# Kernel tuning notes

Hardware: AMD Instinct MI355X
Metric: run time of the kernel (lower is better)

Reference implementation:

```python
import jax, jax.numpy as jnp
import numpy as np

DIM = 1024
NUM_HEADS = 16
NUM_KV_HEADS = 2
HEAD_DIM = DIM // NUM_HEADS          # 64
REPEATS = NUM_HEADS // NUM_KV_HEADS  # 8
WINDOW = 256
HALF = WINDOW // 2                   # 128
BATCH, SEQ = 2, 2048


def setup_inputs() -> dict:
    key = jax.random.key(0)
    ks = jax.random.split(key, 9)
    sc = 1.0 / np.sqrt(DIM)
    return {
        "x":  jax.random.normal(ks[0], (BATCH, SEQ, DIM), jnp.float32),
        "Wq": jax.random.normal(ks[1], (DIM, NUM_HEADS * HEAD_DIM), jnp.float32) * sc,
        "bq": jax.random.normal(ks[2], (NUM_HEADS * HEAD_DIM,), jnp.float32) * 0.01,
        "Wk": jax.random.normal(ks[3], (DIM, NUM_KV_HEADS * HEAD_DIM), jnp.float32) * sc,
        "bk": jax.random.normal(ks[4], (NUM_KV_HEADS * HEAD_DIM,), jnp.float32) * 0.01,
        "Wv": jax.random.normal(ks[5], (DIM, NUM_KV_HEADS * HEAD_DIM), jnp.float32) * sc,
        "bv": jax.random.normal(ks[6], (NUM_KV_HEADS * HEAD_DIM,), jnp.float32) * 0.01,
        "Wo": jax.random.normal(ks[7], (DIM, DIM), jnp.float32) * sc,
        "bo": jax.random.normal(ks[8], (DIM,), jnp.float32) * 0.01,
    }


def reference(x, Wq, bq, Wk, bk, Wv, bv, Wo, bo):
    # Training-path GQA sliding-window attention (faithful to the torch module):
    #  - K/V zero-padded by HALF on each side of the sequence; window of size
    #    WINDOW centered on each query position (unfold with step 1).
    #  - NOTE (faithful): the original code builds mask = tril(ones)[-1], which is
    #    an all-ones row, so masked_fill is a no-op -> NO causal mask inside the
    #    window; padded positions contribute score 0 (not -inf) to the softmax.
    #  - NOTE (faithful): the training path does NOT scale scores by 1/sqrt(d).
    b, s, _ = x.shape
    q = (x @ Wq + bq).reshape(b, s, NUM_HEADS, HEAD_DIM).transpose(0, 2, 1, 3)      # [b,H,s,d]
    k = (x @ Wk + bk).reshape(b, s, NUM_KV_HEADS, HEAD_DIM).transpose(0, 2, 1, 3)   # [b,G,s,d]
    v = (x @ Wv + bv).reshape(b, s, NUM_KV_HEADS, HEAD_DIM).transpose(0, 2, 1, 3)

    kp = jnp.pad(k, ((0, 0), (0, 0), (HALF, HALF), (0, 0)))  # [b,G,s+W,d]
    vp = jnp.pad(v, ((0, 0), (0, 0), (HALF, HALF), (0, 0)))

    # window gather indices: window i covers padded positions [i, i+W)
    idx = jnp.arange(s)[:, None] + jnp.arange(WINDOW)[None, :]  # [s,W]
    k_win = kp[:, :, idx]  # [b,G,s,W,d]  (gather at kv-head granularity, not H)
    v_win = vp[:, :, idx]

    # group query heads by kv head: head h -> kv group h // REPEATS
    qg = q.reshape(b, NUM_KV_HEADS, REPEATS, s, HEAD_DIM)        # [b,G,r,s,d]
    scores = jnp.einsum('bgrsd,bgswd->bgrsw', qg, k_win)         # no scaling (faithful)
    probs = jax.nn.softmax(scores, axis=-1)
    out = jnp.einsum('bgrsw,bgswd->bgrsd', probs, v_win)         # [b,G,r,s,d]

    out = out.reshape(b, NUM_HEADS, s, HEAD_DIM).transpose(0, 2, 1, 3).reshape(b, s, DIM)
    return out @ Wo + bo
```

## Files before the change

kernel.cpp:

```cpp
#include <hip/hip_runtime.h>
#include <hip/hip_fp16.h>

typedef _Float16 h16;
typedef __attribute__((ext_vector_type(4))) _Float16 h16x4;
typedef __attribute__((ext_vector_type(8))) _Float16 h16x8;
typedef __attribute__((ext_vector_type(4))) float f32x4;

#define DIM   1024
#define SEQ   2048
#define NKV   2
#define HD    64
#define HALFW 128
#define NQKV  1280
#define KSTG  288
#define KCOLS 272
#define VSTR  312

__global__ void preprocess_kernel(const float* __restrict__ x,
                                  const float* __restrict__ bq,
                                  const float* __restrict__ bk,
                                  const float* __restrict__ bv,
                                  const float* __restrict__ Wq,
                                  const float* __restrict__ Wk,
                                  const float* __restrict__ Wv,
                                  const float* __restrict__ Wo,
                                  h16* __restrict__ xh, float* __restrict__ bqkv,
                                  h16* __restrict__ wqkvt, h16* __restrict__ wot)
{
    __shared__ float tile[32][33];
    const int tid = threadIdx.x;
    const int blk = blockIdx.x;
    if (blk < 2048) {
        int i = blk * 256 + tid;
        size_t base = (size_t)i * 8;
        float4 a = *(const float4*)(x + base);
        float4 b = *(const float4*)(x + base + 4);
        h16x8 o = { (h16)a.x,(h16)a.y,(h16)a.z,(h16)a.w,
                    (h16)b.x,(h16)b.y,(h16)b.z,(h16)b.w };
        *(h16x8*)(xh + base) = o;
        if (i < NQKV) {
            float v = (i < DIM) ? bq[i] : (i < DIM+128 ? bk[i-DIM] : bv[i-DIM-128]);
            bqkv[i] = v;
        }
        return;
    }
    const int tx = tid & 31, ty = tid >> 5;
    if (blk < 2048 + 1280) {
        int bid = blk - 2048;
        int n0 = (bid % 40) * 32, k0 = (bid / 40) * 32;
        const float* src; int ldn, noff;
        if (n0 < DIM)          { src = Wq; ldn = DIM; noff = n0; }
        else if (n0 < DIM+128) { src = Wk; ldn = 128; noff = n0 - DIM; }
        else                   { src = Wv; ldn = 128; noff = n0 - DIM - 128; }
#pragma unroll
        for (int i = 0; i < 4; ++i)
            tile[ty + 8*i][tx] = src[(size_t)(k0 + ty + 8*i)*ldn + noff + tx];
        __syncthreads();
#pragma unroll
        for (int i = 0; i < 4; ++i)
            wqkvt[(size_t)(n0 + ty + 8*i)*DIM + k0 + tx] = (h16)tile[tx][ty + 8*i];
    } else {
        int bid = blk - 3328;
        int n0 = (bid % 32) * 32, k0 = (bid / 32) * 32;
#pragma unroll
        for (int i = 0; i < 4; ++i)
            tile[ty + 8*i][tx] = Wo[(size_t)(k0 + ty + 8*i)*DIM + n0 + tx];
        __syncthreads();
#pragma unroll
        for (int i = 0; i < 4; ++i)
            wot[(size_t)(n0 + ty + 8*i)*DIM + k0 + tx] = (h16)tile[tx][ty + 8*i];
    }
}

__global__ void vtrans_kernel(const h16* __restrict__ v, h16* __restrict__ vt)
{
    __shared__ h16 tile[32][33];
    const int s0 = blockIdx.x * 32, d0 = blockIdx.y * 32, bg = blockIdx.z;
    const h16* src = v  + (size_t)bg * SEQ * HD;
    h16*       dst = vt + (size_t)bg * SEQ * HD;
    const int tx = threadIdx.x & 31, ty = threadIdx.x >> 5;
#pragma unroll
    for (int i = 0; i < 4; ++i)
        tile[ty + 8*i][tx] = src[(size_t)(s0 + ty + 8*i)*HD + d0 + tx];
    __syncthreads();
#pragma unroll
    for (int i = 0; i < 4; ++i)
        dst[(size_t)(d0 + ty + 8*i)*SEQ + s0 + tx] = tile[tx][ty + 8*i];
}

template<int MODE>
__global__ __launch_bounds__(256, 2)
void gemm_kernel(const h16* __restrict__ A, const h16* __restrict__ Bt,
                 const float* __restrict__ bias,
                 h16* __restrict__ qo, h16* __restrict__ ko, h16* __restrict__ vo,
                 float* __restrict__ co, int K, int nx)
{
    __shared__ __align__(16) h16 As[2][128*64];
    __shared__ __align__(16) h16 Bs[2][128*64];
    const int nwg = gridDim.x, bid = blockIdx.x;
    const int q8 = nwg >> 3, r8 = nwg & 7, xcd = bid & 7, off = bid >> 3;
    const int wg = (xcd < r8 ? xcd*(q8+1) : r8*(q8+1) + (xcd-r8)*q8) + off;
    const int m0 = (wg / nx) * 128, n0 = (wg % nx) * 128;
    const int tid = threadIdx.x, lane = tid & 63, wid = tid >> 6;
    const int wr = wid >> 1, wc = wid & 1;
    f32x4 acc[4][4] = {};

    auto stage = [&](int buf, int kk) {
#pragma unroll
        for (int i = 0; i < 4; ++i) {
            int slot = i*256 + tid;
            int row = slot >> 3;
            int scol = ((slot & 7) ^ (row & 7)) * 8;
            __builtin_amdgcn_global_load_lds(
                (const __attribute__((address_space(1))) void*)(A + (size_t)(m0 + row)*K + kk + scol),
                (__attribute__((address_space(3))) void*)(&As[buf][slot*8]), 16, 0, 0);
            __builtin_amdgcn_global_load_lds(
                (const __attribute__((address_space(1))) void*)(Bt + (size_t)(n0 + row)*K + kk + scol),
                (__attribute__((address_space(3))) void*)(&Bs[buf][slot*8]), 16, 0, 0);
        }
    };
    auto compute = [&](int buf) {
#pragma unroll
        for (int k2 = 0; k2 < 2; ++k2) {
            h16x8 a[4], b[4];
#pragma unroll
            for (int mi = 0; mi < 4; ++mi) {
                int row = wr*64 + mi*16 + (lane & 15);
                int cc = (k2*4 + (lane >> 4)) ^ (row & 7);
                a[mi] = *(const h16x8*)(&As[buf][row*64 + cc*8]);
            }
#pragma unroll
            for (int ni = 0; ni < 4; ++ni) {
                int row = wc*64 + ni*16 + (lane & 15);
                int cc = (k2*4 + (lane >> 4)) ^ (row & 7);
                b[ni] = *(const h16x8*)(&Bs[buf][row*64 + cc*8]);
            }
#pragma unroll
            for (int mi = 0; mi < 4; ++mi)
#pragma unroll
                for (int ni = 0; ni < 4; ++ni)
                    acc[mi][ni] = __builtin_amdgcn_mfma_f32_16x16x32_f16(a[mi], b[ni], acc[mi][ni], 0, 0, 0);
        }
    };

    const int ns = K >> 6;
    stage(0, 0);
    int cur = 0;
    for (int i = 0; i < ns; ++i) {
        if (i < ns-1) {
            stage(cur ^ 1, (i+1) << 6);
            asm volatile("s_waitcnt vmcnt(8)" ::: "memory");
        } else {
            asm volatile("s_waitcnt vmcnt(0)" ::: "memory");
        }
        __builtin_amdgcn_s_barrier();
        __builtin_amdgcn_sched_barrier(0);
        compute(cur);
        if (i < ns-1) {
            __builtin_amdgcn_s_barrier();
            __builtin_amdgcn_sched_barrier(0);
        }
        cur ^= 1;
    }

#pragma unroll
    for (int ni = 0; ni < 4; ++ni) {
        int n = n0 + wc*64 + ni*16 + (lane & 15);
        float bv = bias[n];
#pragma unroll
        for (int mi = 0; mi < 4; ++mi) {
            int mb = m0 + wr*64 + mi*16 + (lane >> 4)*4;
#pragma unroll
            for (int r = 0; r < 4; ++r) {
                int m = mb + r;
                float v = acc[mi][ni][r] + bv;
                if (MODE == 1) {
                    co[(size_t)m*DIM + n] = v;
                } else {
                    h16 hv = (h16)v;
                    if (n < DIM) {
                        qo[(size_t)m*DIM + n] = hv;
                    } else {
                        int nn = n - DIM;
                        int bi2 = m >> 11, s = m & 2047;
                        int g = (nn & 127) >> 6, d = nn & 63;
                        h16* dstp = (nn < 128) ? ko : vo;
                        dstp[(((size_t)(bi2*NKV + g))*SEQ + s)*HD + d] = hv;
                    }
                }
            }
        }
    }
}

__global__ __launch_bounds__(512)
void attn_kernel(const h16* __restrict__ qb, const h16* __restrict__ kb,
                 const h16* __restrict__ vtb, h16* __restrict__ ob)
{
    extern __shared__ char smem[];
    h16* Ks  = (h16*)smem;
    h16* Vts = (h16*)(smem + 36864);
    h16* Ps  = (h16*)(smem + 36864 + 39936);
    const int tid = threadIdx.x, lane = tid & 63, wid = tid >> 6;
    const int qt = blockIdx.x, g = blockIdx.y, bi = blockIdx.z;
    const int s0 = qt * 32;
    const size_t kvbase = ((size_t)(bi*NKV + g)) * SEQ * HD;

    for (int slot = tid; slot < KSTG*8; slot += 512) {
        int row = slot >> 3, cc = slot & 7;
        int kpos = s0 - HALFW + row;
        h16x8 val = {0,0,0,0,0,0,0,0};
        if (kpos >= 0 && kpos < SEQ)
            val = *(const h16x8*)(kb + kvbase + (size_t)kpos*HD + cc*8);
        *(h16x8*)(Ks + row*64 + ((cc ^ (row & 7)) * 8)) = val;
    }
    for (int slot = tid; slot < 64*38; slot += 512) {
        int row = slot / 38, cc = slot - row*38;
        int c0 = cc * 8;
        int kp0 = s0 - HALFW + c0;
        const h16* vrow = vtb + kvbase + (size_t)row*SEQ;
        h16x8 val = {0,0,0,0,0,0,0,0};
        if (kp0 >= 0 && kp0 + 8 <= SEQ) {
            val = *(const h16x8*)(vrow + kp0);
        } else {
#pragma unroll
            for (int j = 0; j < 8; ++j) {
                int kp = kp0 + j;
                val[j] = (kp >= 0 && kp < SEQ) ? vrow[kp] : (h16)0;
            }
        }
        *(h16x8*)(Vts + row*VSTR + c0) = val;
    }
    h16* P = Ps + wid * 16 * VSTR;
    for (int i = lane; i < 256; i += 64)
        P[(i >> 4)*VSTR + KCOLS + (i & 15)] = (h16)0;
    __syncthreads();

    const int h = g*8 + wid;
    const int colbase = lane & 15;
    const int rowbase = (lane >> 4) * 4;
    const int kg = rowbase;

    for (int strip = 0; strip < 2; ++strip) {
        const int ss0 = s0 + strip*16;
        h16x8 aq[2];
#pragma unroll
        for (int c = 0; c < 2; ++c)
            aq[c] = *(const h16x8*)(qb + ((size_t)(bi*SEQ + ss0 + colbase))*DIM
                                    + h*HD + c*32 + (lane >> 4)*8);

        f32x4 sc[17];
        __builtin_amdgcn_s_setprio(1);
#pragma unroll
        for (int t = 0; t < 17; ++t) {
            f32x4 z = {0.f,0.f,0.f,0.f};
#pragma unroll
            for (int c = 0; c < 2; ++c) {
                int key = strip*16 + t*16 + colbase;
                h16x8 kf = *(const h16x8*)(Ks + key*64 + (((c*4 + (lane >> 4)) ^ (key & 7)) * 8));
                z = __builtin_amdgcn_mfma_f32_16x16x32_f16(kf, aq[c], z, 0, 0, 0);
            }
            sc[t] = z;
        }
        __builtin_amdgcn_s_setprio(0);

        float mx = -1e30f;
#pragma unroll
        for (int r = 0; r < 4; ++r) {
            float v0  = (kg + r >= colbase) ? sc[0][r]  : -1e30f;
            float v16 = (kg + r <  colbase) ? sc[16][r] : -1e30f;
            sc[0][r] = v0; sc[16][r] = v16;
            mx = fmaxf(mx, fmaxf(v0, v16));
        }
#pragma unroll
        for (int t = 1; t < 16; ++t)
#pragma unroll
            for (int r = 0; r < 4; ++r) mx = fmaxf(mx, sc[t][r]);
        mx = fmaxf(mx, __shfl_xor(mx, 16));
        mx = fmaxf(mx, __shfl_xor(mx, 32));
        float sum = 0.f;
#pragma unroll
        for (int t = 0; t < 17; ++t)
#pragma unroll
            for (int r = 0; r < 4; ++r) {
                float p = __expf(sc[t][r] - mx);
                sc[t][r] = p;
                sum += p;
            }
        sum += __shfl_xor(sum, 16);
        sum += __shfl_xor(sum, 32);
        float inv = 1.0f / sum;

#pragma unroll
        for (int t = 0; t < 17; ++t) {
            h16x4 pk = { (h16)(sc[t][0]*inv), (h16)(sc[t][1]*inv),
                         (h16)(sc[t][2]*inv), (h16)(sc[t][3]*inv) };
            *(h16x4*)(P + colbase*VSTR + t*16 + kg) = pk;
        }

        f32x4 ao[4] = {};
        __builtin_amdgcn_s_setprio(1);
#pragma unroll
        for (int c = 0; c < 9; ++c) {
            h16x8 pa = *(const h16x8*)(P + colbase*VSTR + c*32 + (lane >> 4)*8);
            int vcol = strip*16 + c*32 + (lane >> 4)*8;
#pragma unroll
            for (int t2 = 0; t2 < 4; ++t2) {
                h16x8 vb = *(const h16x8*)(Vts + (t2*16 + colbase)*VSTR + vcol);
                ao[t2] = __builtin_amdgcn_mfma_f32_16x16x32_f16(pa, vb, ao[t2], 0, 0, 0);
            }
        }
        __builtin_amdgcn_s_setprio(0);
#pragma unroll
        for (int t2 = 0; t2 < 4; ++t2)
#pragma unroll
            for (int r = 0; r < 4; ++r)
                ob[((size_t)(bi*SEQ + ss0 + rowbase + r))*DIM + h*HD + t2*16 + colbase]
                    = (h16)ao[t2][r];
        if (strip == 0) __syncthreads();
    }
}

extern "C" void kernel_launch(void* const* d_in, const int* in_sizes, int n_in,
                              void* d_out, int out_size, void* d_ws, size_t ws_size,
                              hipStream_t stream)
{
    const float* x  = (const float*)d_in[0];
    const float* Wq = (const float*)d_in[1];
    const float* bq = (const float*)d_in[2];
    const float* Wk = (const float*)d_in[3];
    const float* bk = (const float*)d_in[4];
    const float* Wv = (const float*)d_in[5];
    const float* bv = (const float*)d_in[6];
    const float* Wo = (const float*)d_in[7];
    const float* bo = (const float*)d_in[8];
    float* out = (float*)d_out;
    char* ws = (char*)d_ws;

    h16*   xh    = (h16*)(ws);
    h16*   wqkvt = (h16*)(ws + 8388608);
    h16*   wot   = (h16*)(ws + 11010048);
    float* bqkv  = (float*)(ws + 13107200);
    h16*   q_b   = (h16*)(ws + 13112320);
    h16*   k_b   = (h16*)(ws + 21500928);
    h16*   vt_b  = (h16*)(ws + 22549504);
    h16*   att_b = (h16*)(ws + 23598080);
    h16*   v_b   = att_b;

    preprocess_kernel<<<4352, 256, 0, stream>>>(x, bq, bk, bv, Wq, Wk, Wv, Wo,
                                                xh, bqkv, wqkvt, wot);
    gemm_kernel<0><<<320, 256, 0, stream>>>(xh, wqkvt, bqkv,
                                            q_b, k_b, v_b, nullptr, DIM, 10);
    vtrans_kernel<<<dim3(64, 2, 4), 256, 0, stream>>>(v_b, vt_b);
    hipFuncSetAttribute((const void*)attn_kernel,
                        hipFuncAttributeMaxDynamicSharedMemorySize, 156672);
    attn_kernel<<<dim3(64,2,2), 512, 156672, stream>>>(q_b, k_b, vt_b, att_b);
    gemm_kernel<1><<<256, 256, 0, stream>>>(att_b, wot, bo,
                                            nullptr, nullptr, nullptr, out, DIM, 8);
}
```

Before: 73.52 us.

## Retile GEMMs to 512-thread blocks with triple-buffered LDS; fold log2e into Q

The GEMM kernel now runs 512 threads per block with 8 waves, each owning a 32xBN/2 tile. It uses triple-buffered dynamic LDS with two stages in flight, and an XCD-aware mapping that gives 256 blocks for both GEMMs. The QKV GEMM uses a 160-wide N tile (staged as 192 rows) so that 1280 columns fit in 256 blocks, which removes the partial wave of 320 blocks. Separately, Wq and bq are prescaled by log2(e) so the softmax can use exp2f instead of __expf. The cost is more LDS per block and a B-stage that over-fetches 32 rows past the tile.

Result: faster. 68.82 us (-6.4%).

```diff
diff --git a/kernel.cpp b/kernel.cpp
--- a/kernel.cpp
+++ b/kernel.cpp
@@ -15,6 +15,7 @@
 #define KSTG  288
 #define KCOLS 272
 #define VSTR  312
+#define LOG2E 1.4426950408889634f
 
 __global__ void preprocess_kernel(const float* __restrict__ x,
                                   const float* __restrict__ bq,
@@ -39,7 +40,8 @@
                     (h16)b.x,(h16)b.y,(h16)b.z,(h16)b.w };
         *(h16x8*)(xh + base) = o;
         if (i < NQKV) {
-            float v = (i < DIM) ? bq[i] : (i < DIM+128 ? bk[i-DIM] : bv[i-DIM-128]);
+            float v = (i < DIM) ? bq[i] * LOG2E
+                                : (i < DIM+128 ? bk[i-DIM] : bv[i-DIM-128]);
             bqkv[i] = v;
         }
         return;
@@ -48,13 +50,13 @@
     if (blk < 2048 + 1280) {
         int bid = blk - 2048;
         int n0 = (bid % 40) * 32, k0 = (bid / 40) * 32;
-        const float* src; int ldn, noff;
-        if (n0 < DIM)          { src = Wq; ldn = DIM; noff = n0; }
-        else if (n0 < DIM+128) { src = Wk; ldn = 128; noff = n0 - DIM; }
-        else                   { src = Wv; ldn = 128; noff = n0 - DIM - 128; }
+        const float* src; int ldn, noff; float scl;
+        if (n0 < DIM)          { src = Wq; ldn = DIM; noff = n0; scl = LOG2E; }
+        else if (n0 < DIM+128) { src = Wk; ldn = 128; noff = n0 - DIM; scl = 1.f; }
+        else                   { src = Wv; ldn = 128; noff = n0 - DIM - 128; scl = 1.f; }
 #pragma unroll
         for (int i = 0; i < 4; ++i)
-            tile[ty + 8*i][tx] = src[(size_t)(k0 + ty + 8*i)*ldn + noff + tx];
+            tile[ty + 8*i][tx] = src[(size_t)(k0 + ty + 8*i)*ldn + noff + tx] * scl;
         __syncthreads();
 #pragma unroll
         for (int i = 0; i < 4; ++i)
@@ -88,88 +90,106 @@
         dst[(size_t)(d0 + ty + 8*i)*SEQ + s0 + tx] = tile[tx][ty + 8*i];
 }
 
-template<int MODE>
-__global__ __launch_bounds__(256, 2)
+template<int MODE, int BN, int BSTG>
+__global__ __launch_bounds__(512)
 void gemm_kernel(const h16* __restrict__ A, const h16* __restrict__ Bt,
                  const float* __restrict__ bias,
                  h16* __restrict__ qo, h16* __restrict__ ko, h16* __restrict__ vo,
-                 float* __restrict__ co, int K, int nx)
-{
-    __shared__ __align__(16) h16 As[2][128*64];
-    __shared__ __align__(16) h16 Bs[2][128*64];
-    const int nwg = gridDim.x, bid = blockIdx.x;
-    const int q8 = nwg >> 3, r8 = nwg & 7, xcd = bid & 7, off = bid >> 3;
-    const int wg = (xcd < r8 ? xcd*(q8+1) : r8*(q8+1) + (xcd-r8)*q8) + off;
-    const int m0 = (wg / nx) * 128, n0 = (wg % nx) * 128;
+                 float* __restrict__ co, int K)
+{
+    constexpr int NI   = BN / 32;
+    constexpr int ABUF = 128 * 64;
+    constexpr int BBUF = BSTG * 64;
+    constexpr int BUFSZ = ABUF + BBUF;
+    extern __shared__ __align__(16) h16 lds[];
+
+    const int bid = blockIdx.x;
+    const int wg = (bid & 7) * 32 + (bid >> 3);
+    const int m0 = (wg >> 3) * 128, n0 = (wg & 7) * BN;
     const int tid = threadIdx.x, lane = tid & 63, wid = tid >> 6;
     const int wr = wid >> 1, wc = wid & 1;
-    f32x4 acc[4][4] = {};
+    f32x4 acc[2][NI] = {};
 
     auto stage = [&](int buf, int kk) {
-#pragma unroll
-        for (int i = 0; i < 4; ++i) {
-            int slot = i*256 + tid;
+        h16* Ab = lds + buf * BUFSZ;
+        h16* Bb = Ab + ABUF;
+#pragma unroll
+        for (int i = 0; i < 2; ++i) {
+            int slot = i*512 + tid;
             int row = slot >> 3;
             int scol = ((slot & 7) ^ (row & 7)) * 8;
             __builtin_amdgcn_global_load_lds(
                 (const __attribute__((address_space(1))) void*)(A + (size_t)(m0 + row)*K + kk + scol),
-                (__attribute__((address_space(3))) void*)(&As[buf][slot*8]), 16, 0, 0);
+                (__attribute__((address_space(3))) void*)(Ab + slot*8), 16, 0, 0);
+        }
+#pragma unroll
+        for (int i = 0; i < BSTG/64; ++i) {
+            int slot = i*512 + tid;
+            int row = slot >> 3;
+            int scol = ((slot & 7) ^ (row & 7)) * 8;
             __builtin_amdgcn_global_load_lds(
                 (const __attribute__((address_space(1))) void*)(Bt + (size_t)(n0 + row)*K + kk + scol),
-                (__attribute__((address_space(3))) void*)(&Bs[buf][slot*8]), 16, 0, 0);
+                (__attribute__((address_space(3))) void*)(Bb + slot*8), 16, 0, 0);
         }
     };
     auto compute = [&](int buf) {
+        const h16* Ab = lds + buf * BUFSZ;
+        const h16* Bb = Ab + ABUF;
 #pragma unroll
         for (int k2 = 0; k2 < 2; ++k2) {
-            h16x8 a[4], b[4];
-#pragma unroll
-            for (int mi = 0; mi < 4; ++mi) {
-                int row = wr*64 + mi*16 + (lane & 15);
+            h16x8 a[2], b[NI];
+#pragma unroll
+            for (int mi = 0; mi < 2; ++mi) {
+                int row = wr*32 + mi*16 + (lane & 15);
                 int cc = (k2*4 + (lane >> 4)) ^ (row & 7);
-                a[mi] = *(const h16x8*)(&As[buf][row*64 + cc*8]);
-            }
-#pragma unroll
-            for (int ni = 0; ni < 4; ++ni) {
-                int row = wc*64 + ni*16 + (lane & 15);
+                a[mi] = *(const h16x8*)(Ab + row*64 + cc*8);
+            }
+#pragma unroll
+            for (int ni = 0; ni < NI; ++ni) {
+                int row = wc*(BN/2) + ni*16 + (lane & 15);
                 int cc = (k2*4 + (lane >> 4)) ^ (row & 7);
-                b[ni] = *(const h16x8*)(&Bs[buf][row*64 + cc*8]);
-            }
-#pragma unroll
-            for (int mi = 0; mi < 4; ++mi)
-#pragma unroll
-                for (int ni = 0; ni < 4; ++ni)
+                b[ni] = *(const h16x8*)(Bb + row*64 + cc*8);
+            }
+#pragma unroll
+            for (int mi = 0; mi < 2; ++mi)
+#pragma unroll
+                for (int ni = 0; ni < NI; ++ni)
                     acc[mi][ni] = __builtin_amdgcn_mfma_f32_16x16x32_f16(a[mi], b[ni], acc[mi][ni], 0, 0, 0);
         }
     };
 
     const int ns = K >> 6;
     stage(0, 0);
-    int cur = 0;
+    stage(1, 64);
+    int cb = 0, sb = 2;
     for (int i = 0; i < ns; ++i) {
-        if (i < ns-1) {
-            stage(cur ^ 1, (i+1) << 6);
-            asm volatile("s_waitcnt vmcnt(8)" ::: "memory");
+        const int rem = ns - 1 - i;
+        if (i + 2 < ns) { stage(sb, (i+2) << 6); sb = (sb == 2) ? 0 : sb + 1; }
+        if (rem >= 2) {
+            if constexpr (BSTG == 192) asm volatile("s_waitcnt vmcnt(10)" ::: "memory");
+            else                       asm volatile("s_waitcnt vmcnt(8)"  ::: "memory");
+        } else if (rem == 1) {
+            if constexpr (BSTG == 192) asm volatile("s_waitcnt vmcnt(5)" ::: "memory");
+            else                       asm volatile("s_waitcnt vmcnt(4)" ::: "memory");
         } else {
             asm volatile("s_waitcnt vmcnt(0)" ::: "memory");
         }
         __builtin_amdgcn_s_barrier();
         __builtin_amdgcn_sched_barrier(0);
-        compute(cur);
-        if (i < ns-1) {
+        compute(cb); cb = (cb == 2) ? 0 : cb + 1;
+        if (rem) {
             __builtin_amdgcn_s_barrier();
             __builtin_amdgcn_sched_barrier(0);
         }
-        cur ^= 1;
-    }
-
-#pragma unroll
-    for (int ni = 0; ni < 4; ++ni) {
-        int n = n0 + wc*64 + ni*16 + (lane & 15);
+    }
+
+#pragma unroll
+    for (int ni = 0; ni < NI; ++ni) {
+        int n = n0 + wc*(BN/2) + ni*16 + (lane & 15);
         float bv = bias[n];
 #pragma unroll
-        for (int mi = 0; mi < 4; ++mi) {
-            int mb = m0 + wr*64 + mi*16 + (lane >> 4)*4;
+        for (int mi = 0; mi < 2; ++mi) {
+            int mb = m0 + wr*32 + mi*16 + (lane >> 4)*4;
 #pragma unroll
             for (int r = 0; r < 4; ++r) {
                 int m = mb + r;
@@ -283,7 +303,7 @@
         for (int t = 0; t < 17; ++t)
 #pragma unroll
             for (int r = 0; r < 4; ++r) {
-                float p = __expf(sc[t][r] - mx);
+                float p = exp2f(sc[t][r] - mx);
                 sc[t][r] = p;
                 sum += p;
             }
@@ -349,12 +369,16 @@
 
     preprocess_kernel<<<4352, 256, 0, stream>>>(x, bq, bk, bv, Wq, Wk, Wv, Wo,
                                                 xh, bqkv, wqkvt, wot);
-    gemm_kernel<0><<<320, 256, 0, stream>>>(xh, wqkvt, bqkv,
-                                            q_b, k_b, v_b, nullptr, DIM, 10);
+    hipFuncSetAttribute((const void*)(gemm_kernel<0,160,192>),
+                        hipFuncAttributeMaxDynamicSharedMemorySize, 122880);
+    gemm_kernel<0,160,192><<<256, 512, 122880, stream>>>(xh, wqkvt, bqkv,
+                                            q_b, k_b, v_b, nullptr, DIM);
     vtrans_kernel<<<dim3(64, 2, 4), 256, 0, stream>>>(v_b, vt_b);
     hipFuncSetAttribute((const void*)attn_kernel,
                         hipFuncAttributeMaxDynamicSharedMemorySize, 156672);
     attn_kernel<<<dim3(64,2,2), 512, 156672, stream>>>(q_b, k_b, vt_b, att_b);
-    gemm_kernel<1><<<256, 256, 0, stream>>>(att_b, wot, bo,
-                                            nullptr, nullptr, nullptr, out, DIM, 8);
-}
+    hipFuncSetAttribute((const void*)(gemm_kernel<1,128,128>),
+                        hipFuncAttributeMaxDynamicSharedMemorySize, 98304);
+    gemm_kernel<1,128,128><<<256, 512, 98304, stream>>>(att_b, wot, bo,
+                                            nullptr, nullptr, nullptr, out, DIM);
+}
```
